# Optimization experiments

Hardware: AMD Instinct MI355X
Metric: run time of the kernel (lower is better)

Reference implementation:

```python
import jax, jax.numpy as jnp
import numpy as np

D_MODEL = 768
N_HEADS = 12
D_HEAD = D_MODEL // N_HEADS

def setup_inputs() -> dict:
    key = jax.random.key(0)
    ks = jax.random.split(key, 5)
    B, T = 2, 4096
    x = jax.random.normal(ks[0], (B, T, D_MODEL), dtype=jnp.float32)
    s_in = 1.0 / np.sqrt(D_MODEL)
    W_qkv = jax.random.normal(ks[1], (D_MODEL, 3 * D_MODEL), dtype=jnp.float32) * s_in
    b_qkv = jnp.zeros((3 * D_MODEL,), dtype=jnp.float32)
    W_proj = jax.random.normal(ks[2], (D_MODEL, D_MODEL), dtype=jnp.float32) * s_in
    b_proj = jnp.zeros((D_MODEL,), dtype=jnp.float32)
    return {"x": x, "W_qkv": W_qkv, "b_qkv": b_qkv, "W_proj": W_proj, "b_proj": b_proj}

def reference(x, W_qkv, b_qkv, W_proj, b_proj):
    B, T, C = x.shape
    qkv = x @ W_qkv + b_qkv                      # [B,T,3C]
    q, k, v = jnp.split(qkv, 3, axis=-1)
    def heads(t):
        return t.reshape(B, T, N_HEADS, D_HEAD).transpose(0, 2, 1, 3)  # [B,H,T,d]
    q, k, v = heads(q), heads(k), heads(v)
    scale = 1.0 / np.sqrt(D_HEAD)
    att = jnp.einsum('bhqd,bhkd->bhqk', q, k) * scale  # [B,H,T,T]
    causal = jnp.tril(jnp.ones((T, T), dtype=bool))
    att = jnp.where(causal[None, None], att, -jnp.inf)
    att = jax.nn.softmax(att, axis=-1)
    y = jnp.einsum('bhqk,bhkd->bhqd', att, v)          # [B,H,T,d]
    y = y.transpose(0, 2, 1, 3).reshape(B, T, C)
    return y @ W_proj + b_proj
```

## Files before the change

### kernel.cpp

```cpp
#include <hip/hip_runtime.h>
#include <hip/hip_bf16.h>

typedef __bf16 bf16_t;
typedef bf16_t bf16x4 __attribute__((ext_vector_type(4)));
typedef bf16_t bf16x8 __attribute__((ext_vector_type(8)));
typedef float  f32x4  __attribute__((ext_vector_type(4)));

#define TSEQ   4096
#define NBATCH 2
#define DMODEL 768
#define NHEADS 12
#define DHEAD  64
#define NTOK   (NBATCH*TSEQ)
#define NQKV   (3*DMODEL)

#define QSCALE 0.18033688011112042f
#define SMAX 24.0f

__device__ __forceinline__ f32x4 mfma16(bf16x8 a, bf16x8 b, f32x4 c) {
  return __builtin_amdgcn_mfma_f32_16x16x32_bf16(a, b, c, 0, 0, 0);
}

__device__ __forceinline__ void glds16(const bf16_t* g, bf16_t* l) {
  __builtin_amdgcn_global_load_lds(
      (const __attribute__((address_space(1))) void*)g,
      (__attribute__((address_space(3))) void*)l, 16, 0, 0);
}

__global__ __launch_bounds__(256) void k_prep(
    const float* __restrict__ W1, bf16_t* __restrict__ O1,
    const float* __restrict__ W2, bf16_t* __restrict__ O2,
    const float* __restrict__ X, bf16_t* __restrict__ Xb) {
  __shared__ bf16_t tile[64][66];
  int t = blockIdx.x;
  if (t >= 576) {
    const int idx = (t - 576) * 256 + threadIdx.x;
#pragma unroll
    for (int it = 0; it < 2; ++it) {
      const long c = (long)idx + (long)it * 393216;
      const float4 v0 = *(const float4*)(X + c * 8);
      const float4 v1 = *(const float4*)(X + c * 8 + 4);
      bf16x8 o;
      o[0] = (bf16_t)v0.x; o[1] = (bf16_t)v0.y;
      o[2] = (bf16_t)v0.z; o[3] = (bf16_t)v0.w;
      o[4] = (bf16_t)v1.x; o[5] = (bf16_t)v1.y;
      o[6] = (bf16_t)v1.z; o[7] = (bf16_t)v1.w;
      *(bf16x8*)(Xb + c * 8) = o;
    }
    return;
  }
  const float* in; bf16_t* out; int R, C, c0, r0;
  if (t < 432) { in = W1; out = O1; R = DMODEL; C = NQKV;
                 c0 = (t % 36) * 64; r0 = (t / 36) * 64; }
  else { t -= 432; in = W2; out = O2; R = DMODEL; C = DMODEL;
         c0 = (t % 12) * 64; r0 = (t / 12) * 64; }
  const int tid = threadIdx.x;
  const int r = tid >> 2, cb = (tid & 3) * 16;
  const float* ip = in + (long)(r0 + r) * C + c0 + cb;
#pragma unroll
  for (int k = 0; k < 16; k += 4) {
    float4 v = *(const float4*)(ip + k);
    tile[r][cb + k + 0] = (bf16_t)v.x;
    tile[r][cb + k + 1] = (bf16_t)v.y;
    tile[r][cb + k + 2] = (bf16_t)v.z;
    tile[r][cb + k + 3] = (bf16_t)v.w;
  }
  __syncthreads();
  const int c = tid >> 2, rb = (tid & 3) * 16;
  bf16_t* op = out + (long)(c0 + c) * R + r0 + rb;
  bf16x8 v0, v1;
#pragma unroll
  for (int i = 0; i < 8; ++i) { v0[i] = tile[rb + i][c]; v1[i] = tile[rb + 8 + i][c]; }
  *(bf16x8*)(op) = v0;
  *(bf16x8*)(op + 8) = v1;
}

__global__ __launch_bounds__(256) void k_gemm_qkv(
    const bf16_t* __restrict__ Xb, const bf16_t* __restrict__ Bt,
    const float* __restrict__ bias,
    bf16_t* __restrict__ Qo, bf16_t* __restrict__ Ko, bf16_t* __restrict__ Vt) {
  __shared__ __align__(16) bf16_t As[3 * 128 * 32];
  __shared__ __align__(16) bf16_t Bs[3 * 128 * 32];
  const int wave = threadIdx.x >> 6;
  const int lane = threadIdx.x & 63;
  const int quad = lane >> 4;
  const int l16  = lane & 15;
  const int m0 = blockIdx.x * 128;
  const int n0 = blockIdx.y * 128;

  const int srow4  = lane >> 2;
  const int schunk = (lane & 3) ^ ((lane >> 3) & 3);
  const bf16_t* a0 = Xb + (long)(m0 + wave * 32 + srow4) * DMODEL + schunk * 8;
  const bf16_t* b0 = Bt + (long)(n0 + wave * 32 + srow4) * DMODEL + schunk * 8;

  f32x4 acc[2][8] = {};

  auto stage = [&](int ks) {
    const int koff = ks * 32;
    bf16_t* Ax = As + (ks % 3) * (128 * 32);
    bf16_t* Bx = Bs + (ks % 3) * (128 * 32);
    glds16(a0 + koff,               Ax + (wave * 32) * 32);
    glds16(a0 + 16 * DMODEL + koff, Ax + (wave * 32 + 16) * 32);
    glds16(b0 + koff,               Bx + (wave * 32) * 32);
    glds16(b0 + 16 * DMODEL + koff, Bx + (wave * 32 + 16) * 32);
  };

  const int NS = DMODEL / 32;
  stage(0);
  stage(1);
  asm volatile("s_waitcnt vmcnt(4)" ::: "memory");
  __builtin_amdgcn_s_barrier();
  __builtin_amdgcn_sched_barrier(0);

  const int sw = (l16 >> 1) & 3;
  for (int ks = 0; ks < NS; ++ks) {
    if (ks + 2 < NS) stage(ks + 2);
    const bf16_t* Ap = As + (ks % 3) * (128 * 32);
    const bf16_t* Bp = Bs + (ks % 3) * (128 * 32);

    bf16x8 af0 = *(const bf16x8*)(Ap + (wave * 32 + l16) * 32 + ((quad ^ sw) << 3));
    bf16x8 af1 = *(const bf16x8*)(Ap + (wave * 32 + 16 + l16) * 32 + ((quad ^ sw) << 3));
#pragma unroll
    for (int nt = 0; nt < 8; ++nt) {
      bf16x8 bfm = *(const bf16x8*)(Bp + (nt * 16 + l16) * 32 + ((quad ^ sw) << 3));
      acc[0][nt] = mfma16(af0, bfm, acc[0][nt]);
      acc[1][nt] = mfma16(af1, bfm, acc[1][nt]);
    }

    if (ks + 1 < NS) {
      if (ks + 2 < NS) {
        asm volatile("s_waitcnt vmcnt(4)" ::: "memory");
      } else {
        asm volatile("s_waitcnt vmcnt(0)" ::: "memory");
      }
      __builtin_amdgcn_s_barrier();
      __builtin_amdgcn_sched_barrier(0);
    }
  }

#pragma unroll
  for (int s = 0; s < 2; ++s)
#pragma unroll
    for (int nt = 0; nt < 8; ++nt) {
      const int n = n0 + nt * 16 + l16;
      const float bv = bias[n];
      const int mb = m0 + wave * 32 + s * 16 + quad * 4;
      const int b = mb >> 12;
      const int t = mb & 4095;
      if (n < DMODEL) {
        const int h = n >> 6, d = n & 63;
        bf16_t* qp = Qo + (((long)(b * NHEADS + h) * TSEQ + t) << 6) + d;
#pragma unroll
        for (int j = 0; j < 4; ++j)
          qp[(long)j << 6] = (bf16_t)((acc[s][nt][j] + bv) * QSCALE);
      } else if (n < 2 * DMODEL) {
        const int n2 = n - DMODEL, h = n2 >> 6, d = n2 & 63;
        bf16_t* kp = Ko + (((long)(b * NHEADS + h) * TSEQ + t) << 6) + d;
#pragma unroll
        for (int j = 0; j < 4; ++j)
          kp[(long)j << 6] = (bf16_t)(acc[s][nt][j] + bv);
      } else {
        const int n2 = n - 2 * DMODEL, h = n2 >> 6, d = n2 & 63;
        bf16x4 v;
#pragma unroll
        for (int j = 0; j < 4; ++j) v[j] = (bf16_t)(acc[s][nt][j] + bv);
        *(bf16x4*)(Vt + ((long)(b * NHEADS + h) * DHEAD + d) * TSEQ + t) = v;
      }
    }
}

__global__ __launch_bounds__(256) void k_combine(
    const bf16_t* __restrict__ P0, const bf16_t* __restrict__ P1,
    const float* __restrict__ L0, const float* __restrict__ L1,
    bf16_t* __restrict__ Ab) {
  const int bh = blockIdx.x;
  const int t  = blockIdx.y * 32 + (threadIdx.x >> 3);
  const int d0 = (threadIdx.x & 7) * 8;
  const long lidx = (long)bh * TSEQ + t;
  const float li = 1.f / (L0[lidx] + L1[lidx]);
  const long pidx = (lidx << 6) + d0;
  bf16x8 a = *(const bf16x8*)(P0 + pidx);
  bf16x8 b = *(const bf16x8*)(P1 + pidx);
  bf16x8 o;
#pragma unroll
  for (int j = 0; j < 8; ++j)
    o[j] = (bf16_t)(((float)a[j] + (float)b[j]) * li);
  const int bb = bh / NHEADS, h = bh % NHEADS;
  *(bf16x8*)(Ab + (long)(bb * TSEQ + t) * DMODEL + h * 64 + d0) = o;
}

__global__ __launch_bounds__(256, 3) void k_gemm_proj(
    const bf16_t* __restrict__ Ab, const bf16_t* __restrict__ Bt,
    const float* __restrict__ bias, float* __restrict__ out) {
  __shared__ __align__(16) bf16_t As[2 * 64 * 64];
  __shared__ __align__(16) bf16_t Bs[2 * 128 * 64];
  const int wave = threadIdx.x >> 6;
  const int lane = threadIdx.x & 63;
  const int quad = lane >> 4;
  const int l16  = lane & 15;
  const int m0 = blockIdx.x * 64;
  const int n0 = blockIdx.y * 128;

  const int srow8  = lane >> 3;
  const int schunk = (lane & 7) ^ srow8;
  const bf16_t* a0 = Ab + (long)(m0 + wave * 16 + srow8) * DMODEL + schunk * 8;
  const bf16_t* b0 = Bt + (long)(n0 + wave * 32 + srow8) * DMODEL + schunk * 8;

  f32x4 acc[2][4] = {};

  auto stageA = [&](int ks, bf16_t* dst) {
    const int koff = ks * 64;
    glds16(a0 + koff,             dst + (wave * 16) * 64);
    glds16(a0 + 8 * DMODEL + koff, dst + (wave * 16 + 8) * 64);
  };
  auto stageB = [&](int ks, bf16_t* dst) {
    const int koff = ks * 64;
    glds16(b0 + koff,              dst + (wave * 32) * 64);
    glds16(b0 + 8 * DMODEL + koff,  dst + (wave * 32 + 8) * 64);
    glds16(b0 + 16 * DMODEL + koff, dst + (wave * 32 + 16) * 64);
    glds16(b0 + 24 * DMODEL + koff, dst + (wave * 32 + 24) * 64);
  };

  stageA(0, As);
  stageB(0, Bs);
  __syncthreads();

  const int sw8 = l16 & 7;
  const int NS = DMODEL / 64;
  for (int ks = 0; ks < NS; ++ks) {
    const int p = ks & 1;
    if (ks + 1 < NS) {
      stageA(ks + 1, p ? As : As + 64 * 64);
      stageB(ks + 1, p ? Bs : Bs + 128 * 64);
    }
    const bf16_t* Ap = As + p * (64 * 64);
    const bf16_t* Bp = Bs + p * (128 * 64);

    bf16x8 af[4][2], bf[2][2];
#pragma unroll
    for (int kk = 0; kk < 2; ++kk) {
      const int rc = (((kk * 4 + quad) ^ sw8) << 3);
      bf[0][kk] = *(const bf16x8*)(Bp + (wave * 32 + l16) * 64 + rc);
      bf[1][kk] = *(const bf16x8*)(Bp + (wave * 32 + 16 + l16) * 64 + rc);
#pragma unroll
      for (int mf = 0; mf < 4; ++mf)
        af[mf][kk] = *(const bf16x8*)(Ap + (mf * 16 + l16) * 64 + rc);
    }
#pragma unroll
    for (int kk = 0; kk < 2; ++kk)
#pragma unroll
      for (int mf = 0; mf < 4; ++mf) {
        acc[0][mf] = mfma16(af[mf][kk], bf[0][kk], acc[0][mf]);
        acc[1][mf] = mfma16(af[mf][kk], bf[1][kk], acc[1][mf]);
      }
    __syncthreads();
  }

#pragma unroll
  for (int nf = 0; nf < 2; ++nf)
#pragma unroll
    for (int mf = 0; mf < 4; ++mf) {
      const int n = n0 + wave * 32 + nf * 16 + l16;
      const float bv = bias[n];
      const int m = m0 + mf * 16 + quad * 4;
#pragma unroll
      for (int j = 0; j < 4; ++j)
        out[(long)(m + j) * DMODEL + n] = acc[nf][mf][j] + bv;
    }
}

__global__ __launch_bounds__(256, 4) void k_attn(
    const bf16_t* __restrict__ Q, const bf16_t* __restrict__ K,
    const bf16_t* __restrict__ Vt,
    bf16_t* __restrict__ P0, bf16_t* __restrict__ P1,
    float* __restrict__ L0, float* __restrict__ L1) {
  __shared__ __align__(16) bf16_t kbuf[2][64 * 64];
  __shared__ __align__(16) bf16_t vbuf[2][64 * 64];
  const int wave = threadIdx.x >> 6;
  const int lane = threadIdx.x & 63;
  const int quad = lane >> 4;
  const int l16  = lane & 15;
  const int bh = blockIdx.x;
  const int qt = 31 - (blockIdx.y >> 1);
  const int sp = blockIdx.y & 1;
  const int niter = qt + 1;
  const int c0 = sp * niter;
  bf16_t* Pp = sp ? P1 : P0;
  float*  Lp = sp ? L1 : L0;

  const bf16_t* Qh = Q + ((long)bh * TSEQ << 6);
  const bf16_t* Kh = K + ((long)bh * TSEQ << 6);
  const bf16_t* Vh = Vt + (long)bh * DHEAD * TSEQ;

  const int qbase = qt * 128 + wave * 32;

  bf16x8 qf[2][2];
#pragma unroll
  for (int s = 0; s < 2; ++s) {
    const bf16_t* qrow = Qh + ((long)(qbase + s * 16 + l16) << 6);
    qf[s][0] = *(const bf16x8*)(qrow + quad * 8);
    qf[s][1] = *(const bf16x8*)(qrow + 32 + quad * 8);
  }

  f32x4 acc[2][4] = {};
  float lS[2] = {0.f, 0.f};
  const f32x4 minit = {-SMAX, -SMAX, -SMAX, -SMAX};

  const int kperm = ((l16 >> 2) << 3) + (l16 & 3);
  const int swl = l16 & 7;
  const int srow = lane >> 3;
  const int cV = (lane & 7) ^ (srow & 7);
  const int cK0 = (lane & 7) ^ (srow & 3);
  const int cK1 = cK0 ^ 4;
  const int r0a = wave * 16, r0b = wave * 16 + 8;

  {
    const int k00 = c0 << 6;
    glds16(Kh + ((long)(k00 + r0a + srow) << 6) + cK0 * 8, &kbuf[0][r0a * 64]);
    glds16(Kh + ((long)(k00 + r0b + srow) << 6) + cK1 * 8, &kbuf[0][r0b * 64]);
    glds16(Vh + (long)(r0a + srow) * TSEQ + k00 + cV * 8,  &vbuf[0][r0a * 64]);
    glds16(Vh + (long)(r0b + srow) * TSEQ + k00 + cV * 8,  &vbuf[0][r0b * 64]);
  }
  __syncthreads();

  for (int ci = 0; ci < niter; ++ci) {
    const int p = ci & 1;
    const int k0 = (c0 + ci) << 6;
    if (ci + 1 < niter) {
      const int k1 = k0 + 64;
      glds16(Kh + ((long)(k1 + r0a + srow) << 6) + cK0 * 8, &kbuf[1 - p][r0a * 64]);
      glds16(Kh + ((long)(k1 + r0b + srow) << 6) + cK1 * 8, &kbuf[1 - p][r0b * 64]);
      glds16(Vh + (long)(r0a + srow) * TSEQ + k1 + cV * 8,  &vbuf[1 - p][r0a * 64]);
      glds16(Vh + (long)(r0b + srow) * TSEQ + k1 + cV * 8,  &vbuf[1 - p][r0b * 64]);
    }
    const bf16_t* kb = kbuf[p];
    const bf16_t* vb = vbuf[p];

#pragma unroll
    for (int g = 0; g < 2; ++g) {
      const int rw0 = (g * 32 + kperm) * 64;
      const int rw1 = (g * 32 + 4 + kperm) * 64;
      bf16x8 kf00 = *(const bf16x8*)(kb + rw0 + ((quad ^ swl) << 3));
      bf16x8 kf01 = *(const bf16x8*)(kb + rw0 + (((quad + 4) ^ swl) << 3));
      bf16x8 kf10 = *(const bf16x8*)(kb + rw1 + ((quad ^ swl) << 3));
      bf16x8 kf11 = *(const bf16x8*)(kb + rw1 + (((quad + 4) ^ swl) << 3));
      const bool domask = (k0 + g * 32 + 31 > qbase);

      bf16x8 pf[2];
#pragma unroll
      for (int s = 0; s < 2; ++s) {
        f32x4 st0 = minit, st1 = minit;
        st0 = mfma16(kf00, qf[s][0], st0);
        st0 = mfma16(kf01, qf[s][1], st0);
        st1 = mfma16(kf10, qf[s][0], st1);
        st1 = mfma16(kf11, qf[s][1], st1);
        if (domask) {
          const int qS = qbase + s * 16 + l16;
          const int kb0 = k0 + g * 32 + quad * 8;
#pragma unroll
          for (int j = 0; j < 4; ++j) {
            if (kb0 + j > qS)     st0[j] = -1e30f;
            if (kb0 + 4 + j > qS) st1[j] = -1e30f;
          }
        }
        float rs = 0.f;
#pragma unroll
        for (int j = 0; j < 4; ++j) {
          float e0 = __builtin_amdgcn_exp2f(st0[j]);
          float e1 = __builtin_amdgcn_exp2f(st1[j]);
          rs += e0 + e1;
          pf[s][j]     = (bf16_t)e0;
          pf[s][4 + j] = (bf16_t)e1;
        }
        lS[s] += rs;
      }
#pragma unroll
      for (int dt = 0; dt < 4; ++dt) {
        const int row = dt * 16 + l16;
        bf16x8 vf = *(const bf16x8*)(vb + row * 64 + ((((g << 2) + quad) ^ swl) << 3));
#pragma unroll
        for (int s = 0; s < 2; ++s)
          acc[s][dt] = mfma16(vf, pf[s], acc[s][dt]);
      }
    }
    __syncthreads();
  }

#pragma unroll
  for (int s = 0; s < 2; ++s) {
    lS[s] += __shfl_xor(lS[s], 16);
    lS[s] += __shfl_xor(lS[s], 32);
  }
#pragma unroll
  for (int s = 0; s < 2; ++s) {
    const int qS = qbase + s * 16 + l16;
    bf16_t* prow = Pp + (((long)bh * TSEQ + qS) << 6);
#pragma unroll
    for (int dt = 0; dt < 4; ++dt) {
      bf16x4 w;
#pragma unroll
      for (int j = 0; j < 4; ++j) w[j] = (bf16_t)acc[s][dt][j];
      *(bf16x4*)(prow + dt * 16 + quad * 4) = w;
    }
    if (quad == 0) Lp[(long)bh * TSEQ + qS] = lS[s];
  }
}

extern "C" void kernel_launch(void* const* d_in, const int* in_sizes, int n_in,
                              void* d_out, int out_size, void* d_ws, size_t ws_size,
                              hipStream_t stream) {
  (void)in_sizes; (void)n_in; (void)out_size; (void)ws_size;
  const float* x     = (const float*)d_in[0];
  const float* Wqkv  = (const float*)d_in[1];
  const float* bqkv  = (const float*)d_in[2];
  const float* Wproj = (const float*)d_in[3];
  const float* bproj = (const float*)d_in[4];
  float* out = (float*)d_out;

  char* ws = (char*)d_ws;
  bf16_t* wqkv_t  = (bf16_t*)ws; ws += (long)NQKV * DMODEL * 2;
  bf16_t* wproj_t = (bf16_t*)ws; ws += (long)DMODEL * DMODEL * 2;
  bf16_t* Xb      = (bf16_t*)ws; ws += (long)NTOK * DMODEL * 2;
  bf16_t* Qb      = (bf16_t*)ws; ws += (long)NTOK * DMODEL * 2;
  bf16_t* Kb      = (bf16_t*)ws; ws += (long)NTOK * DMODEL * 2;
  bf16_t* Vtb     = (bf16_t*)ws; ws += (long)NTOK * DMODEL * 2;
  bf16_t* P0b     = (bf16_t*)ws; ws += (long)NTOK * DMODEL * 2;
  bf16_t* P1b     = (bf16_t*)ws; ws += (long)NTOK * DMODEL * 2;
  bf16_t* Abb     = (bf16_t*)ws; ws += (long)NTOK * DMODEL * 2;
  float*  L0b     = (float*)ws;  ws += (long)NHEADS * NBATCH * TSEQ * 4;
  float*  L1b     = (float*)ws;  ws += (long)NHEADS * NBATCH * TSEQ * 4;

  k_prep<<<576 + 1536, 256, 0, stream>>>(Wqkv, wqkv_t, Wproj, wproj_t, x, Xb);
  k_gemm_qkv<<<dim3(NTOK / 128, NQKV / 128), 256, 0, stream>>>(Xb, wqkv_t, bqkv, Qb, Kb, Vtb);
  k_attn<<<dim3(NBATCH * NHEADS, 64), 256, 0, stream>>>(Qb, Kb, Vtb, P0b, P1b, L0b, L1b);
  k_combine<<<dim3(NBATCH * NHEADS, TSEQ / 32), 256, 0, stream>>>(
      P0b, P1b, L0b, L1b, Abb);
  k_gemm_proj<<<dim3(NTOK / 64, DMODEL / 128), 256, 0, stream>>>(
      Abb, wproj_t, bproj, out);
}
```

Measured before the change: 216.5 us.

## Use BK=64 double-buffered QKV GEMM and set MFMA priority in attention

```diff
diff --git a/kernel.cpp b/kernel.cpp
--- a/kernel.cpp
+++ b/kernel.cpp
@@ -79,8 +79,8 @@
     const bf16_t* __restrict__ Xb, const bf16_t* __restrict__ Bt,
     const float* __restrict__ bias,
     bf16_t* __restrict__ Qo, bf16_t* __restrict__ Ko, bf16_t* __restrict__ Vt) {
-  __shared__ __align__(16) bf16_t As[3 * 128 * 32];
-  __shared__ __align__(16) bf16_t Bs[3 * 128 * 32];
+  __shared__ __align__(16) bf16_t As[2 * 128 * 64];
+  __shared__ __align__(16) bf16_t Bs[2 * 128 * 64];
   const int wave = threadIdx.x >> 6;
   const int lane = threadIdx.x & 63;
   const int quad = lane >> 4;
@@ -88,54 +88,47 @@
   const int m0 = blockIdx.x * 128;
   const int n0 = blockIdx.y * 128;
 
-  const int srow4  = lane >> 2;
-  const int schunk = (lane & 3) ^ ((lane >> 3) & 3);
-  const bf16_t* a0 = Xb + (long)(m0 + wave * 32 + srow4) * DMODEL + schunk * 8;
-  const bf16_t* b0 = Bt + (long)(n0 + wave * 32 + srow4) * DMODEL + schunk * 8;
+  const int srow8  = lane >> 3;
+  const int schunk = (lane & 7) ^ srow8;
+  const bf16_t* a0 = Xb + (long)(m0 + wave * 32 + srow8) * DMODEL + schunk * 8;
+  const bf16_t* b0 = Bt + (long)(n0 + wave * 32 + srow8) * DMODEL + schunk * 8;
 
   f32x4 acc[2][8] = {};
 
-  auto stage = [&](int ks) {
-    const int koff = ks * 32;
-    bf16_t* Ax = As + (ks % 3) * (128 * 32);
-    bf16_t* Bx = Bs + (ks % 3) * (128 * 32);
-    glds16(a0 + koff,               Ax + (wave * 32) * 32);
-    glds16(a0 + 16 * DMODEL + koff, Ax + (wave * 32 + 16) * 32);
-    glds16(b0 + koff,               Bx + (wave * 32) * 32);
-    glds16(b0 + 16 * DMODEL + koff, Bx + (wave * 32 + 16) * 32);
+  auto stage = [&](int ks, bf16_t* Ax, bf16_t* Bx) {
+    const int koff = ks * 64;
+#pragma unroll
+    for (int sl = 0; sl < 4; ++sl) {
+      glds16(a0 + (long)sl * 8 * DMODEL + koff, Ax + (wave * 32 + sl * 8) * 64);
+      glds16(b0 + (long)sl * 8 * DMODEL + koff, Bx + (wave * 32 + sl * 8) * 64);
+    }
   };
 
-  const int NS = DMODEL / 32;
-  stage(0);
-  stage(1);
-  asm volatile("s_waitcnt vmcnt(4)" ::: "memory");
-  __builtin_amdgcn_s_barrier();
-  __builtin_amdgcn_sched_barrier(0);
-
-  const int sw = (l16 >> 1) & 3;
+  stage(0, As, Bs);
+  __syncthreads();
+
+  const int sw8 = l16 & 7;
+  const int NS = DMODEL / 64;
   for (int ks = 0; ks < NS; ++ks) {
-    if (ks + 2 < NS) stage(ks + 2);
-    const bf16_t* Ap = As + (ks % 3) * (128 * 32);
-    const bf16_t* Bp = Bs + (ks % 3) * (128 * 32);
-
-    bf16x8 af0 = *(const bf16x8*)(Ap + (wave * 32 + l16) * 32 + ((quad ^ sw) << 3));
-    bf16x8 af1 = *(const bf16x8*)(Ap + (wave * 32 + 16 + l16) * 32 + ((quad ^ sw) << 3));
-#pragma unroll
-    for (int nt = 0; nt < 8; ++nt) {
-      bf16x8 bfm = *(const bf16x8*)(Bp + (nt * 16 + l16) * 32 + ((quad ^ sw) << 3));
-      acc[0][nt] = mfma16(af0, bfm, acc[0][nt]);
-      acc[1][nt] = mfma16(af1, bfm, acc[1][nt]);
-    }
-
-    if (ks + 1 < NS) {
-      if (ks + 2 < NS) {
-        asm volatile("s_waitcnt vmcnt(4)" ::: "memory");
-      } else {
-        asm volatile("s_waitcnt vmcnt(0)" ::: "memory");
+    const int p = ks & 1;
+    if (ks + 1 < NS)
+      stage(ks + 1, p ? As : As + 128 * 64, p ? Bs : Bs + 128 * 64);
+    const bf16_t* Ap = As + p * (128 * 64);
+    const bf16_t* Bp = Bs + p * (128 * 64);
+
+#pragma unroll
+    for (int kk = 0; kk < 2; ++kk) {
+      const int rc = ((kk * 4 + quad) ^ sw8) << 3;
+      bf16x8 af0 = *(const bf16x8*)(Ap + (wave * 32 + l16) * 64 + rc);
+      bf16x8 af1 = *(const bf16x8*)(Ap + (wave * 32 + 16 + l16) * 64 + rc);
+#pragma unroll
+      for (int nt = 0; nt < 8; ++nt) {
+        bf16x8 bfm = *(const bf16x8*)(Bp + (nt * 16 + l16) * 64 + rc);
+        acc[0][nt] = mfma16(af0, bfm, acc[0][nt]);
+        acc[1][nt] = mfma16(af1, bfm, acc[1][nt]);
       }
-      __builtin_amdgcn_s_barrier();
-      __builtin_amdgcn_sched_barrier(0);
-    }
+    }
+    __syncthreads();
   }
 
 #pragma unroll
@@ -350,10 +343,12 @@
 #pragma unroll
       for (int s = 0; s < 2; ++s) {
         f32x4 st0 = minit, st1 = minit;
+        __builtin_amdgcn_s_setprio(1);
         st0 = mfma16(kf00, qf[s][0], st0);
         st0 = mfma16(kf01, qf[s][1], st0);
         st1 = mfma16(kf10, qf[s][0], st1);
         st1 = mfma16(kf11, qf[s][1], st1);
+        __builtin_amdgcn_s_setprio(0);
         if (domask) {
           const int qS = qbase + s * 16 + l16;
           const int kb0 = k0 + g * 32 + quad * 8;
@@ -374,6 +369,7 @@
         }
         lS[s] += rs;
       }
+      __builtin_amdgcn_s_setprio(1);
 #pragma unroll
       for (int dt = 0; dt < 4; ++dt) {
         const int row = dt * 16 + l16;
@@ -382,6 +378,7 @@
         for (int s = 0; s < 2; ++s)
           acc[s][dt] = mfma16(vf, pf[s], acc[s][dt]);
       }
+      __builtin_amdgcn_s_setprio(0);
     }
     __syncthreads();
   }
```

Result: no change. 219.0 us (+1.2%).
